# Optimization experiments

Hardware: AMD Instinct MI355X
Metric: run time of the kernel (lower is better)

## Reference

```python
import jax, jax.numpy as jnp
import numpy as np
from jax import lax

C = 64
B, H, W = 4, 192, 192


def conv2d(x, w, b):
    # x: [B,C,H,W], w: [O,I,3,3] (OIHW), stride 1, pad 1
    y = lax.conv_general_dilated(x, w, (1, 1), ((1, 1), (1, 1)),
                                 dimension_numbers=("NCHW", "OIHW", "NCHW"))
    return y + b[None, :, None, None]


def csm(x, w1, b1, w2, b2):
    # residual block: conv3x3 -> relu -> conv3x3 + skip
    return x + conv2d(jax.nn.relu(conv2d(x, w1, b1)), w2, b2)


def setup_inputs() -> dict:
    key = jax.random.key(0)
    ks = jax.random.split(key, 12)
    s = 1.0 / np.sqrt(C * 9)
    def cw(k):
        return jax.random.uniform(k, (C, C, 3, 3), jnp.float32, -s, s)
    def cb(k):
        return jax.random.uniform(k, (C,), jnp.float32, -s, s)
    return {
        "low1": jax.random.normal(ks[0], (B, C, H, W), jnp.float32),
        "low2": jax.random.normal(ks[1], (B, C, H, W), jnp.float32),
        "fe1_w1": cw(ks[2]), "fe1_b1": cb(ks[3]),
        "fe1_w2": cw(ks[4]), "fe1_b2": cb(ks[5]),
        "fe2_w1": cw(ks[6]), "fe2_b1": cb(ks[7]),
        "fe2_w2": cw(ks[8]), "fe2_b2": cb(ks[9]),
        "conv_w": cw(ks[10]), "conv_b": cb(ks[11]),
    }


def reference(low1, low2, fe1_w1, fe1_b1, fe1_w2, fe1_b2,
              fe2_w1, fe2_b1, fe2_w2, fe2_b2, conv_w, conv_b):
    Q1 = conv2d(csm(low1, fe1_w1, fe1_b1, fe1_w2, fe1_b2), conv_w, conv_b)
    K1 = conv2d(csm(low2, fe1_w1, fe1_b1, fe1_w2, fe1_b2), conv_w, conv_b)
    Q2 = conv2d(csm(low1, fe2_w1, fe2_b1, fe2_w2, fe2_b2), conv_w, conv_b)
    K2 = conv2d(csm(low2, fe2_w1, fe2_b1, fe2_w2, fe2_b2), conv_w, conv_b)

    # per-row cross-width scores: [B,H,W,W] (no scaling; softmax then relu)
    score1 = jax.nn.relu(jax.nn.softmax(jnp.einsum("bchw,bchv->bhwv", Q1, K1), axis=-1))
    score2 = jax.nn.relu(jax.nn.softmax(jnp.einsum("bchw,bchv->bhwv", Q2, K2), axis=-1))

    def apply_score(score, feat):
        # out[b,c,h,w] = sum_v score[b,h,w,v] * feat[b,c,h,v]
        return jnp.einsum("bhwv,bchv->bchw", score, feat)

    def apply_score_T(score, feat):
        # out[b,c,h,w] = sum_v score[b,h,v,w] * feat[b,c,h,v]
        return jnp.einsum("bhvw,bchv->bchw", score, feat)

    right2left1 = apply_score(score1, low2)
    right2left2 = apply_score(score2, low2)
    left2right1 = apply_score_T(score1, low1)
    left2right2 = apply_score_T(score2, low1)
    left2right2left = apply_score(score2, left2right1)
    right2left2right = apply_score_T(score2, right2left1)

    left = low1 + right2left1 + right2left2 + left2right2left
    right = low2 + left2right1 + left2right2 + right2left2right
    return (left, right)
```

## Files before the change

### kernel.cpp

```cpp
#include <hip/hip_runtime.h>
#include <stdint.h>

#define NB 4
#define NC 64
#define NH 192
#define NW 192

typedef __attribute__((ext_vector_type(8))) short bf16x8;
typedef __attribute__((ext_vector_type(4))) float f32x4;
typedef unsigned short u16;
typedef unsigned int u32;

__device__ inline float bf2f(u16 x){ u32 u = ((u32)x) << 16; return __builtin_bit_cast(float, u); }
__device__ inline u16 f2bf(float f){ u32 u = __builtin_bit_cast(u32, f); u32 r = u + 0x7fffu + ((u >> 16) & 1u); return (u16)(r >> 16); }
__device__ inline bf16x8 packf8(float4 a, float4 b){
  bf16x8 r;
  r[0]=(short)f2bf(a.x); r[1]=(short)f2bf(a.y); r[2]=(short)f2bf(a.z); r[3]=(short)f2bf(a.w);
  r[4]=(short)f2bf(b.x); r[5]=(short)f2bf(b.y); r[6]=(short)f2bf(b.z); r[7]=(short)f2bf(b.w);
  return r;
}

__global__ void wxform_k(const float* __restrict__ w0, const float* __restrict__ w1,
                         const float* __restrict__ w2, const float* __restrict__ w3,
                         const float* __restrict__ w4, u16* __restrict__ out){
  int idx = blockIdx.x * 256 + threadIdx.x;
  if (idx >= 5 * 36864) return;
  int t = idx / 36864, e = idx % 36864;
  int r = e >> 12, rem = e & 4095, co = rem >> 6, ci = rem & 63;
  const float* src = (t == 0) ? w0 : (t == 1) ? w1 : (t == 2) ? w2 : (t == 3) ? w3 : w4;
  out[idx] = f2bf(src[co * 576 + ci * 9 + r]);
}

__global__ __launch_bounds__(192) void nchw2nhwc_k(const float* __restrict__ in, u16* __restrict__ out){
  int bh = blockIdx.x; int b = bh / NH, h = bh % NH;
  int w = threadIdx.x;
  u16 v[64];
  const float* p = in + ((size_t)b * NC * NH + h) * NW + w;
#pragma unroll
  for (int c = 0; c < 64; ++c) v[c] = f2bf(p[(size_t)c * NH * NW]);
  uint4* q4 = (uint4*)(out + ((size_t)bh * NW + w) * NC);
#pragma unroll
  for (int i = 0; i < 8; ++i){
    uint4 t;
    t.x = (u32)v[i*8+0] | ((u32)v[i*8+1] << 16);
    t.y = (u32)v[i*8+2] | ((u32)v[i*8+3] << 16);
    t.z = (u32)v[i*8+4] | ((u32)v[i*8+5] << 16);
    t.w = (u32)v[i*8+6] | ((u32)v[i*8+7] << 16);
    q4[i] = t;
  }
}

__global__ __launch_bounds__(256) void bf2f_k(const u16* __restrict__ in, float* __restrict__ out){
  int i = blockIdx.x * 256 + threadIdx.x;
  uint4 v = ((const uint4*)in)[i];
  float4 f0, f1;
  f0.x = bf2f((u16)(v.x & 0xffff)); f0.y = bf2f((u16)(v.x >> 16));
  f0.z = bf2f((u16)(v.y & 0xffff)); f0.w = bf2f((u16)(v.y >> 16));
  f1.x = bf2f((u16)(v.z & 0xffff)); f1.y = bf2f((u16)(v.z >> 16));
  f1.z = bf2f((u16)(v.w & 0xffff)); f1.w = bf2f((u16)(v.w >> 16));
  ((float4*)out)[2*i]   = f0;
  ((float4*)out)[2*i+1] = f1;
}

__global__ __launch_bounds__(256) void conv3_k(const u16* __restrict__ in, const u16* __restrict__ wt,
    const float* __restrict__ bias, const u16* __restrict__ skip, u16* __restrict__ out, int relu){
  __shared__ __align__(16) u16 xr[3][98 * 72];
  int blk0 = blockIdx.x;
  int blk = (blk0 & 7) * 64 + (blk0 >> 3);
  int wh = blk & 1;
  int strip = blk >> 1;
  int g0 = strip * 3;
  int b = g0 / NH, h0 = g0 % NH;
  int wstart = wh * 96;
  int tid = threadIdx.x;
  int wvv = tid >> 6, lane = tid & 63, l15 = lane & 15, qd = lane >> 4;
  int mh = wvv >> 1, wq = wvv & 1;

#define STAGE(hh_) do { \
    int hh = (hh_); \
    int slot = ((hh % 3) + 3) % 3; \
    bool rowok = (hh >= 0) && (hh < NH); \
    const u16* src = in + (((size_t)b * NH + (rowok ? hh : 0)) * NW) * 64; \
    for (int k2 = tid; k2 < 784; k2 += 256){ \
      int x = k2 >> 3, part = k2 & 7; \
      int w = wstart - 1 + x; \
      uint4 val = make_uint4(0,0,0,0); \
      if (rowok && w >= 0 && w < NW) val = *(const uint4*)(src + (size_t)w * 64 + part * 8); \
      *(uint4*)&xr[slot][x * 72 + part * 8] = val; \
    } \
  } while(0)

  STAGE(h0 - 1);
  STAGE(h0);
  for (int j = 0; j < 3; ++j){
    int h = h0 + j;
    STAGE(h + 1);
    __syncthreads();
    f32x4 acc[2][3];
#pragma unroll
    for (int mt = 0; mt < 2; ++mt)
#pragma unroll
      for (int nt = 0; nt < 3; ++nt) acc[mt][nt] = (f32x4){0.f,0.f,0.f,0.f};
#pragma unroll
    for (int r = 0; r < 9; ++r){
      int ky = r / 3, kx = r % 3;
      int hs = h - 1 + ky;
      const u16* xbase = xr[((hs % 3) + 3) % 3];
#pragma unroll
      for (int ks = 0; ks < 2; ++ks){
        int ci = ks * 32 + qd * 8;
        const u16* wp_ = wt + r * 4096 + ci;
        bf16x8 a0 = *(const bf16x8*)(wp_ + (mh * 32 + l15) * 64);
        bf16x8 a1 = *(const bf16x8*)(wp_ + (mh * 32 + 16 + l15) * 64);
#pragma unroll
        for (int nt = 0; nt < 3; ++nt){
          int x = wq * 48 + nt * 16 + l15 + kx;
          bf16x8 bfr = *(const bf16x8*)&xbase[x * 72 + ci];
          acc[0][nt] = __builtin_amdgcn_mfma_f32_16x16x32_bf16(a0, bfr, acc[0][nt], 0, 0, 0);
          acc[1][nt] = __builtin_amdgcn_mfma_f32_16x16x32_bf16(a1, bfr, acc[1][nt], 0, 0, 0);
        }
      }
    }
    size_t rowbase = ((size_t)(b * NH + h)) * NW * 64;
#pragma unroll
    for (int mt = 0; mt < 2; ++mt){
      int co0 = mh * 32 + mt * 16 + qd * 4;
      float4 bb = *(const float4*)(bias + co0);
#pragma unroll
      for (int nt = 0; nt < 3; ++nt){
        int w = wstart + wq * 48 + nt * 16 + l15;
        size_t o = rowbase + (size_t)w * 64 + co0;
        float v0 = acc[mt][nt][0] + bb.x, v1 = acc[mt][nt][1] + bb.y;
        float v2 = acc[mt][nt][2] + bb.z, v3 = acc[mt][nt][3] + bb.w;
        if (relu){ v0 = fmaxf(v0,0.f); v1 = fmaxf(v1,0.f); v2 = fmaxf(v2,0.f); v3 = fmaxf(v3,0.f); }
        if (skip){
          uint2 ss = *(const uint2*)(skip + o);
          v0 += bf2f((u16)(ss.x & 0xffff)); v1 += bf2f((u16)(ss.x >> 16));
          v2 += bf2f((u16)(ss.y & 0xffff)); v3 += bf2f((u16)(ss.y >> 16));
        }
        uint2 st;
        st.x = (u32)f2bf(v0) | ((u32)f2bf(v1) << 16);
        st.y = (u32)f2bf(v2) | ((u32)f2bf(v3) << 16);
        *(uint2*)(out + o) = st;
      }
    }
    __syncthreads();
  }
#undef STAGE
}

template<int XYF32>
__global__ __launch_bounds__(256) void attn_k(const u16* __restrict__ Q, const u16* __restrict__ K,
    const void* __restrict__ Xv, const void* __restrict__ Yv,
    u16* __restrict__ outA, u16* __restrict__ outB){
  __shared__ __align__(16) u16 P[192 * 200];
  int bh = blockIdx.x, b = bh / NH, h = bh % NH;
  int tid = threadIdx.x, wv = tid >> 6, lane = tid & 63, l15 = lane & 15, qd = lane >> 4;
  size_t rowo = (size_t)bh * NW * 64;
  const u16* Qr = Q + rowo; const u16* Kr = K + rowo;
  const size_t CS = (size_t)NH * NW;
  size_t xb0 = (size_t)b * 64 * CS + (size_t)h * NW;
  const float* Xf = (const float*)Xv; const float* Yf = (const float*)Yv;
  const u16* Xb = (const u16*)Xv; const u16* Yb = (const u16*)Yv;

#pragma unroll 1
  for (int mi = 0; mi < 3; ++mi){
    int mt = wv * 3 + mi;
    f32x4 s[12];
#pragma unroll
    for (int nt = 0; nt < 12; ++nt) s[nt] = (f32x4){0,0,0,0};
#pragma unroll
    for (int ks = 0; ks < 2; ++ks){
      bf16x8 aq = *(const bf16x8*)(Qr + (mt * 16 + l15) * 64 + ks * 32 + qd * 8);
#pragma unroll
      for (int nt = 0; nt < 12; ++nt){
        bf16x8 bk = *(const bf16x8*)(Kr + (nt * 16 + l15) * 64 + ks * 32 + qd * 8);
        s[nt] = __builtin_amdgcn_mfma_f32_16x16x32_bf16(aq, bk, s[nt], 0, 0, 0);
      }
    }
#pragma unroll
    for (int rg = 0; rg < 4; ++rg){
      float mx = -1e30f;
#pragma unroll
      for (int nt = 0; nt < 12; ++nt) mx = fmaxf(mx, s[nt][rg]);
      mx = fmaxf(mx, __shfl_xor(mx, 1));
      mx = fmaxf(mx, __shfl_xor(mx, 2));
      mx = fmaxf(mx, __shfl_xor(mx, 4));
      mx = fmaxf(mx, __shfl_xor(mx, 8));
      float sum = 0.f;
#pragma unroll
      for (int nt = 0; nt < 12; ++nt){ float ev = __expf(s[nt][rg] - mx); s[nt][rg] = ev; sum += ev; }
      sum += __shfl_xor(sum, 1);
      sum += __shfl_xor(sum, 2);
      sum += __shfl_xor(sum, 4);
      sum += __shfl_xor(sum, 8);
      float inv = 1.f / sum;
      int w = mt * 16 + qd * 4 + rg;
#pragma unroll
      for (int nt = 0; nt < 12; ++nt){
        P[w * 200 + nt * 16 + l15] = f2bf(s[nt][rg] * inv);
      }
    }
  }

  {
    f32x4 accA[3][4];
#pragma unroll
    for (int ni = 0; ni < 3; ++ni)
#pragma unroll
      for (int mt = 0; mt < 4; ++mt) accA[ni][mt] = (f32x4){0,0,0,0};
#pragma unroll 1
    for (int ks = 0; ks < 6; ++ks){
      int v0 = ks * 32 + qd * 8;
      bf16x8 aX[4];
#pragma unroll
      for (int mt = 0; mt < 4; ++mt){
        int c = mt * 16 + l15;
        size_t off = xb0 + (size_t)c * CS + v0;
        if (XYF32){
          float4 x0 = *(const float4*)(Xf + off), x1 = *(const float4*)(Xf + off + 4);
          aX[mt] = packf8(x0, x1);
        } else {
          aX[mt] = *(const bf16x8*)(Xb + off);
        }
      }
#pragma unroll
      for (int ni = 0; ni < 3; ++ni){
        int wrow = (wv * 3 + ni) * 16 + l15;
        bf16x8 bP = *(const bf16x8*)&P[wrow * 200 + v0];
#pragma unroll
        for (int mt = 0; mt < 4; ++mt){
          accA[ni][mt] = __builtin_amdgcn_mfma_f32_16x16x32_bf16(aX[mt], bP, accA[ni][mt], 0, 0, 0);
        }
      }
    }
#pragma unroll
    for (int ni = 0; ni < 3; ++ni){
      int w = (wv * 3 + ni) * 16 + l15;
#pragma unroll
      for (int mt = 0; mt < 4; ++mt){
#pragma unroll
        for (int rg = 0; rg < 4; ++rg){
          int c = mt * 16 + qd * 4 + rg;
          size_t o = xb0 + (size_t)c * CS + w;
          float ra = XYF32 ? Yf[o] : bf2f(Yb[o]);
          outA[o] = f2bf(accA[ni][mt][rg] + ra);
        }
      }
    }
  }

  __syncthreads();

  {
    int r = tid >> 4, c = tid & 15;
#pragma unroll 1
    for (int TI = 0; TI < 12; ++TI){
      if (c > r){
        u16 a = P[(TI*16 + r)*200 + TI*16 + c];
        u16 d = P[(TI*16 + c)*200 + TI*16 + r];
        P[(TI*16 + r)*200 + TI*16 + c] = d;
        P[(TI*16 + c)*200 + TI*16 + r] = a;
      }
      int TJ = TI + 1;
      for (; TJ + 1 < 12; TJ += 2){
        u16 a0 = P[(TI*16 + r)*200 + TJ*16 + c];
        u16 b0 = P[(TJ*16 + c)*200 + TI*16 + r];
        u16 a1 = P[(TI*16 + r)*200 + (TJ+1)*16 + c];
        u16 b1 = P[((TJ+1)*16 + c)*200 + TI*16 + r];
        P[(TI*16 + r)*200 + TJ*16 + c] = b0;
        P[(TJ*16 + c)*200 + TI*16 + r] = a0;
        P[(TI*16 + r)*200 + (TJ+1)*16 + c] = b1;
        P[((TJ+1)*16 + c)*200 + TI*16 + r] = a1;
      }
      if (TJ < 12){
        u16 a0 = P[(TI*16 + r)*200 + TJ*16 + c];
        u16 b0 = P[(TJ*16 + c)*200 + TI*16 + r];
        P[(TI*16 + r)*200 + TJ*16 + c] = b0;
        P[(TJ*16 + c)*200 + TI*16 + r] = a0;
      }
    }
  }

  __syncthreads();

  {
    f32x4 accB[3][4];
#pragma unroll
    for (int ni = 0; ni < 3; ++ni)
#pragma unroll
      for (int mt = 0; mt < 4; ++mt) accB[ni][mt] = (f32x4){0,0,0,0};
#pragma unroll 1
    for (int ks = 0; ks < 6; ++ks){
      int v0 = ks * 32 + qd * 8;
      bf16x8 aY[4];
#pragma unroll
      for (int mt = 0; mt < 4; ++mt){
        int c = mt * 16 + l15;
        size_t off = xb0 + (size_t)c * CS + v0;
        if (XYF32){
          float4 y0 = *(const float4*)(Yf + off), y1 = *(const float4*)(Yf + off + 4);
          aY[mt] = packf8(y0, y1);
        } else {
          aY[mt] = *(const bf16x8*)(Yb + off);
        }
      }
#pragma unroll
      for (int ni = 0; ni < 3; ++ni){
        int wrow = (wv * 3 + ni) * 16 + l15;
        bf16x8 bPt = *(const bf16x8*)&P[wrow * 200 + v0];
#pragma unroll
        for (int mt = 0; mt < 4; ++mt){
          accB[ni][mt] = __builtin_amdgcn_mfma_f32_16x16x32_bf16(aY[mt], bPt, accB[ni][mt], 0, 0, 0);
        }
      }
    }
#pragma unroll
    for (int ni = 0; ni < 3; ++ni){
      int w = (wv * 3 + ni) * 16 + l15;
#pragma unroll
      for (int mt = 0; mt < 4; ++mt){
#pragma unroll
        for (int rg = 0; rg < 4; ++rg){
          int c = mt * 16 + qd * 4 + rg;
          size_t o = xb0 + (size_t)c * CS + w;
          float rb = XYF32 ? Xf[o] : bf2f(Xb[o]);
          outB[o] = f2bf(accB[ni][mt][rg] + rb);
        }
      }
    }
  }
}

extern "C" void kernel_launch(void* const* d_in, const int* in_sizes, int n_in,
                              void* d_out, int out_size, void* d_ws, size_t ws_size,
                              hipStream_t stream){
  const float* low1 = (const float*)d_in[0];
  const float* low2 = (const float*)d_in[1];
  const float* b11 = (const float*)d_in[3];
  const float* b12 = (const float*)d_in[5];
  const float* b21 = (const float*)d_in[7];
  const float* b22 = (const float*)d_in[9];
  const float* bcv = (const float*)d_in[11];
  const size_t BUF = (size_t)NB * NH * NW * NC;
  u16* WT = (u16*)d_ws;
  u16* s1 = WT + 184320;
  u16* s2 = s1 + BUF;
  u16* o1 = (u16*)d_out;
  u16* o2 = o1 + BUF;
  u16* o3 = o1 + 2 * BUF;
  u16* o4 = o1 + 3 * BUF;
  float* outL = (float*)d_out;
  float* outR = outL + BUF;

  wxform_k<<<dim3(720), dim3(256), 0, stream>>>(
      (const float*)d_in[2], (const float*)d_in[4], (const float*)d_in[6],
      (const float*)d_in[8], (const float*)d_in[10], WT);
  nchw2nhwc_k<<<dim3(NB * NH), dim3(192), 0, stream>>>(low1, o1);
  nchw2nhwc_k<<<dim3(NB * NH), dim3(192), 0, stream>>>(low2, o2);

#define CONV(in_, wti, bias_, skip_, out_, relu_) \
  conv3_k<<<dim3(512), dim3(256), 0, stream>>>(in_, WT + (wti) * 36864, bias_, skip_, out_, relu_)

  CONV(o1, 0, b11, (const u16*)nullptr, o3, 1);
  CONV(o3, 1, b12, o1, o4, 0);
  CONV(o4, 4, bcv, (const u16*)nullptr, s1, 0);
  CONV(o2, 0, b11, (const u16*)nullptr, o3, 1);
  CONV(o3, 1, b12, o2, o4, 0);
  CONV(o4, 4, bcv, (const u16*)nullptr, s2, 0);
  attn_k<1><<<dim3(NB * NH), dim3(256), 0, stream>>>(s1, s2, (const void*)low2, (const void*)low1, o3, o4);
  CONV(o1, 2, b21, (const u16*)nullptr, s1, 1);
  CONV(s1, 3, b22, o1, s2, 0);
  CONV(s2, 4, bcv, (const u16*)nullptr, o1, 0);
  CONV(o2, 2, b21, (const u16*)nullptr, s1, 1);
  CONV(s1, 3, b22, o2, s2, 0);
  CONV(s2, 4, bcv, (const u16*)nullptr, o2, 0);
  attn_k<0><<<dim3(NB * NH), dim3(256), 0, stream>>>(o1, o2, (const void*)o4, (const void*)o3, s1, s2);
  bf2f_k<<<dim3((int)(BUF / 8 / 256)), dim3(256), 0, stream>>>(s1, outL);
  bf2f_k<<<dim3((int)(BUF / 8 / 256)), dim3(256), 0, stream>>>(s2, outR);
#undef CONV
}
```

Baseline: 604.3 us.

## Drop LDS row staging in conv; one output row per block, read inputs from global

The conv kernel no longer stages three input rows into shared memory with barriers. Each block now computes a single output row half, and the MFMA B fragments load directly from global memory with boundary masking. The grid triples to 1536 blocks and launch bounds request 4 blocks per CU. This removes the LDS traffic and __syncthreads stalls and raises occupancy, but gives up the reuse of staged rows across 3 output rows and kx shifts, so it leans more on L1/L2 for the repeated loads.

Measured after the change: 1.288 ms. 113% more time.

```diff
diff --git a/kernel.cpp b/kernel.cpp
--- a/kernel.cpp
+++ b/kernel.cpp
@@ -62,50 +62,34 @@
   ((float4*)out)[2*i+1] = f1;
 }
 
-__global__ __launch_bounds__(256) void conv3_k(const u16* __restrict__ in, const u16* __restrict__ wt,
+__global__ __launch_bounds__(256, 4) void conv3_k(const u16* __restrict__ in, const u16* __restrict__ wt,
     const float* __restrict__ bias, const u16* __restrict__ skip, u16* __restrict__ out, int relu){
-  __shared__ __align__(16) u16 xr[3][98 * 72];
   int blk0 = blockIdx.x;
-  int blk = (blk0 & 7) * 64 + (blk0 >> 3);
+  int blk = (blk0 & 7) * 192 + (blk0 >> 3);
   int wh = blk & 1;
-  int strip = blk >> 1;
-  int g0 = strip * 3;
-  int b = g0 / NH, h0 = g0 % NH;
+  int bh = blk >> 1;
+  int b = bh / NH, h = bh % NH;
   int wstart = wh * 96;
   int tid = threadIdx.x;
-  int wvv = tid >> 6, lane = tid & 63, l15 = lane & 15, qd = lane >> 4;
-  int mh = wvv >> 1, wq = wvv & 1;
-
-#define STAGE(hh_) do { \
-    int hh = (hh_); \
-    int slot = ((hh % 3) + 3) % 3; \
-    bool rowok = (hh >= 0) && (hh < NH); \
-    const u16* src = in + (((size_t)b * NH + (rowok ? hh : 0)) * NW) * 64; \
-    for (int k2 = tid; k2 < 784; k2 += 256){ \
-      int x = k2 >> 3, part = k2 & 7; \
-      int w = wstart - 1 + x; \
-      uint4 val = make_uint4(0,0,0,0); \
-      if (rowok && w >= 0 && w < NW) val = *(const uint4*)(src + (size_t)w * 64 + part * 8); \
-      *(uint4*)&xr[slot][x * 72 + part * 8] = val; \
-    } \
-  } while(0)
-
-  STAGE(h0 - 1);
-  STAGE(h0);
-  for (int j = 0; j < 3; ++j){
-    int h = h0 + j;
-    STAGE(h + 1);
-    __syncthreads();
-    f32x4 acc[2][3];
-#pragma unroll
-    for (int mt = 0; mt < 2; ++mt)
-#pragma unroll
-      for (int nt = 0; nt < 3; ++nt) acc[mt][nt] = (f32x4){0.f,0.f,0.f,0.f};
-#pragma unroll
-    for (int r = 0; r < 9; ++r){
-      int ky = r / 3, kx = r % 3;
-      int hs = h - 1 + ky;
-      const u16* xbase = xr[((hs % 3) + 3) % 3];
+  int wv = tid >> 6, lane = tid & 63, l15 = lane & 15, qd = lane >> 4;
+  int mh = wv >> 1, wq = wv & 1;
+
+  f32x4 acc[2][3];
+#pragma unroll
+  for (int mt = 0; mt < 2; ++mt)
+#pragma unroll
+    for (int nt = 0; nt < 3; ++nt) acc[mt][nt] = (f32x4){0.f,0.f,0.f,0.f};
+
+  const bf16x8 zero8 = {0,0,0,0,0,0,0,0};
+
+#pragma unroll 1
+  for (int ky = 0; ky < 3; ++ky){
+    int hs = h - 1 + ky;
+    bool rowok = (hs >= 0) && (hs < NH);
+    const u16* srow = in + (((size_t)b * NH + (rowok ? hs : 0)) * NW) * 64;
+#pragma unroll
+    for (int kx = 0; kx < 3; ++kx){
+      int r = ky * 3 + kx;
 #pragma unroll
       for (int ks = 0; ks < 2; ++ks){
         int ci = ks * 32 + qd * 8;
@@ -114,39 +98,39 @@
         bf16x8 a1 = *(const bf16x8*)(wp_ + (mh * 32 + 16 + l15) * 64);
 #pragma unroll
         for (int nt = 0; nt < 3; ++nt){
-          int x = wq * 48 + nt * 16 + l15 + kx;
-          bf16x8 bfr = *(const bf16x8*)&xbase[x * 72 + ci];
+          int x = wstart + wq * 48 + nt * 16 + l15 + kx - 1;
+          bf16x8 bfr = zero8;
+          if (rowok && x >= 0 && x < NW) bfr = *(const bf16x8*)(srow + (size_t)x * 64 + ci);
           acc[0][nt] = __builtin_amdgcn_mfma_f32_16x16x32_bf16(a0, bfr, acc[0][nt], 0, 0, 0);
           acc[1][nt] = __builtin_amdgcn_mfma_f32_16x16x32_bf16(a1, bfr, acc[1][nt], 0, 0, 0);
         }
       }
     }
-    size_t rowbase = ((size_t)(b * NH + h)) * NW * 64;
-#pragma unroll
-    for (int mt = 0; mt < 2; ++mt){
-      int co0 = mh * 32 + mt * 16 + qd * 4;
-      float4 bb = *(const float4*)(bias + co0);
-#pragma unroll
-      for (int nt = 0; nt < 3; ++nt){
-        int w = wstart + wq * 48 + nt * 16 + l15;
-        size_t o = rowbase + (size_t)w * 64 + co0;
-        float v0 = acc[mt][nt][0] + bb.x, v1 = acc[mt][nt][1] + bb.y;
-        float v2 = acc[mt][nt][2] + bb.z, v3 = acc[mt][nt][3] + bb.w;
-        if (relu){ v0 = fmaxf(v0,0.f); v1 = fmaxf(v1,0.f); v2 = fmaxf(v2,0.f); v3 = fmaxf(v3,0.f); }
-        if (skip){
-          uint2 ss = *(const uint2*)(skip + o);
-          v0 += bf2f((u16)(ss.x & 0xffff)); v1 += bf2f((u16)(ss.x >> 16));
-          v2 += bf2f((u16)(ss.y & 0xffff)); v3 += bf2f((u16)(ss.y >> 16));
-        }
-        uint2 st;
-        st.x = (u32)f2bf(v0) | ((u32)f2bf(v1) << 16);
-        st.y = (u32)f2bf(v2) | ((u32)f2bf(v3) << 16);
-        *(uint2*)(out + o) = st;
-      }
-    }
-    __syncthreads();
-  }
-#undef STAGE
+  }
+
+  size_t rowbase = ((size_t)(b * NH + h)) * NW * 64;
+#pragma unroll
+  for (int mt = 0; mt < 2; ++mt){
+    int co0 = mh * 32 + mt * 16 + qd * 4;
+    float4 bb = *(const float4*)(bias + co0);
+#pragma unroll
+    for (int nt = 0; nt < 3; ++nt){
+      int w = wstart + wq * 48 + nt * 16 + l15;
+      size_t o = rowbase + (size_t)w * 64 + co0;
+      float v0 = acc[mt][nt][0] + bb.x, v1 = acc[mt][nt][1] + bb.y;
+      float v2 = acc[mt][nt][2] + bb.z, v3 = acc[mt][nt][3] + bb.w;
+      if (relu){ v0 = fmaxf(v0,0.f); v1 = fmaxf(v1,0.f); v2 = fmaxf(v2,0.f); v3 = fmaxf(v3,0.f); }
+      if (skip){
+        uint2 ss = *(const uint2*)(skip + o);
+        v0 += bf2f((u16)(ss.x & 0xffff)); v1 += bf2f((u16)(ss.x >> 16));
+        v2 += bf2f((u16)(ss.y & 0xffff)); v3 += bf2f((u16)(ss.y >> 16));
+      }
+      uint2 st;
+      st.x = (u32)f2bf(v0) | ((u32)f2bf(v1) << 16);
+      st.y = (u32)f2bf(v2) | ((u32)f2bf(v3) << 16);
+      *(uint2*)(out + o) = st;
+    }
+  }
 }
 
 template<int XYF32>
@@ -360,7 +344,7 @@
   nchw2nhwc_k<<<dim3(NB * NH), dim3(192), 0, stream>>>(low2, o2);
 
 #define CONV(in_, wti, bias_, skip_, out_, relu_) \
-  conv3_k<<<dim3(512), dim3(256), 0, stream>>>(in_, WT + (wti) * 36864, bias_, skip_, out_, relu_)
+  conv3_k<<<dim3(1536), dim3(256), 0, stream>>>(in_, WT + (wti) * 36864, bias_, skip_, out_, relu_)
 
   CONV(o1, 0, b11, (const u16*)nullptr, o3, 1);
   CONV(o3, 1, b12, o1, o4, 0);
```

## Batch paired conv streams into single launches and fuse attention epilogues

Applied to the files above, without the earlier changes.

The conv kernel now handles both feature streams (low1 and low2 paths) in one launch, with 768 blocks that each process 4 rows instead of 3. A launch-bounds occupancy hint of 3 blocks is added, and the number of conv launches drops from twelve to six. The attention kernel keeps both accumulator sets live and writes both outputs in one final epilogue, which allows outputs to alias inputs and lets buffers be reused. The aim is to cut launch overhead, improve GPU fill and amortize halo staging. The cost is more register pressure in the attention kernel and fewer blocks per stream.

New measurement: 671.0 us. 1.11x slower.

```diff
diff --git a/kernel.cpp b/kernel.cpp
--- a/kernel.cpp
+++ b/kernel.cpp
@@ -62,16 +62,24 @@
   ((float4*)out)[2*i+1] = f1;
 }
 
-__global__ __launch_bounds__(256) void conv3_k(const u16* __restrict__ in, const u16* __restrict__ wt,
-    const float* __restrict__ bias, const u16* __restrict__ skip, u16* __restrict__ out, int relu){
+__global__ __launch_bounds__(256, 3) void conv3m_k(
+    const u16* __restrict__ inA, const u16* __restrict__ inB,
+    const u16* __restrict__ wt, const float* __restrict__ bias,
+    const u16* __restrict__ skipA, const u16* __restrict__ skipB,
+    u16* __restrict__ outA, u16* __restrict__ outB, int relu){
   __shared__ __align__(16) u16 xr[3][98 * 72];
   int blk0 = blockIdx.x;
-  int blk = (blk0 & 7) * 64 + (blk0 >> 3);
-  int wh = blk & 1;
-  int strip = blk >> 1;
-  int g0 = strip * 3;
+  int blk = (blk0 & 7) * 96 + (blk0 >> 3);
+  int stream = blk / 384;
+  int r2 = blk % 384;
+  int wh = r2 & 1;
+  int strip = r2 >> 1;
+  int g0 = strip * 4;
   int b = g0 / NH, h0 = g0 % NH;
   int wstart = wh * 96;
+  const u16* in = stream ? inB : inA;
+  const u16* skip = stream ? skipB : skipA;
+  u16* out = stream ? outB : outA;
   int tid = threadIdx.x;
   int wvv = tid >> 6, lane = tid & 63, l15 = lane & 15, qd = lane >> 4;
   int mh = wvv >> 1, wq = wvv & 1;
@@ -92,7 +100,7 @@
 
   STAGE(h0 - 1);
   STAGE(h0);
-  for (int j = 0; j < 3; ++j){
+  for (int j = 0; j < 4; ++j){
     int h = h0 + j;
     STAGE(h + 1);
     __syncthreads();
@@ -203,49 +211,34 @@
     }
   }
 
-  {
-    f32x4 accA[3][4];
-#pragma unroll
-    for (int ni = 0; ni < 3; ++ni)
-#pragma unroll
-      for (int mt = 0; mt < 4; ++mt) accA[ni][mt] = (f32x4){0,0,0,0};
+  f32x4 accA[3][4], accB[3][4];
+#pragma unroll
+  for (int ni = 0; ni < 3; ++ni)
+#pragma unroll
+    for (int mt = 0; mt < 4; ++mt){ accA[ni][mt] = (f32x4){0,0,0,0}; accB[ni][mt] = (f32x4){0,0,0,0}; }
+
 #pragma unroll 1
-    for (int ks = 0; ks < 6; ++ks){
-      int v0 = ks * 32 + qd * 8;
-      bf16x8 aX[4];
+  for (int ks = 0; ks < 6; ++ks){
+    int v0 = ks * 32 + qd * 8;
+    bf16x8 aX[4];
+#pragma unroll
+    for (int mt = 0; mt < 4; ++mt){
+      int c = mt * 16 + l15;
+      size_t off = xb0 + (size_t)c * CS + v0;
+      if (XYF32){
+        float4 x0 = *(const float4*)(Xf + off), x1 = *(const float4*)(Xf + off + 4);
+        aX[mt] = packf8(x0, x1);
+      } else {
+        aX[mt] = *(const bf16x8*)(Xb + off);
+      }
+    }
+#pragma unroll
+    for (int ni = 0; ni < 3; ++ni){
+      int wrow = (wv * 3 + ni) * 16 + l15;
+      bf16x8 bP = *(const bf16x8*)&P[wrow * 200 + v0];
 #pragma unroll
       for (int mt = 0; mt < 4; ++mt){
-        int c = mt * 16 + l15;
-        size_t off = xb0 + (size_t)c * CS + v0;
-        if (XYF32){
-          float4 x0 = *(const float4*)(Xf + off), x1 = *(const float4*)(Xf + off + 4);
-          aX[mt] = packf8(x0, x1);
-        } else {
-          aX[mt] = *(const bf16x8*)(Xb + off);
-        }
-      }
-#pragma unroll
-      for (int ni = 0; ni < 3; ++ni){
-        int wrow = (wv * 3 + ni) * 16 + l15;
-        bf16x8 bP = *(const bf16x8*)&P[wrow * 200 + v0];
-#pragma unroll
-        for (int mt = 0; mt < 4; ++mt){
-          accA[ni][mt] = __builtin_amdgcn_mfma_f32_16x16x32_bf16(aX[mt], bP, accA[ni][mt], 0, 0, 0);
-        }
-      }
-    }
-#pragma unroll
-    for (int ni = 0; ni < 3; ++ni){
-      int w = (wv * 3 + ni) * 16 + l15;
-#pragma unroll
-      for (int mt = 0; mt < 4; ++mt){
-#pragma unroll
-        for (int rg = 0; rg < 4; ++rg){
-          int c = mt * 16 + qd * 4 + rg;
-          size_t o = xb0 + (size_t)c * CS + w;
-          float ra = XYF32 ? Yf[o] : bf2f(Yb[o]);
-          outA[o] = f2bf(accA[ni][mt][rg] + ra);
-        }
+        accA[ni][mt] = __builtin_amdgcn_mfma_f32_16x16x32_bf16(aX[mt], bP, accA[ni][mt], 0, 0, 0);
       }
     }
   }
@@ -284,49 +277,45 @@
 
   __syncthreads();
 
-  {
-    f32x4 accB[3][4];
-#pragma unroll
-    for (int ni = 0; ni < 3; ++ni)
-#pragma unroll
-      for (int mt = 0; mt < 4; ++mt) accB[ni][mt] = (f32x4){0,0,0,0};
 #pragma unroll 1
-    for (int ks = 0; ks < 6; ++ks){
-      int v0 = ks * 32 + qd * 8;
-      bf16x8 aY[4];
+  for (int ks = 0; ks < 6; ++ks){
+    int v0 = ks * 32 + qd * 8;
+    bf16x8 aY[4];
+#pragma unroll
+    for (int mt = 0; mt < 4; ++mt){
+      int c = mt * 16 + l15;
+      size_t off = xb0 + (size_t)c * CS + v0;
+      if (XYF32){
+        float4 y0 = *(const float4*)(Yf + off), y1 = *(const float4*)(Yf + off + 4);
+        aY[mt] = packf8(y0, y1);
+      } else {
+        aY[mt] = *(const bf16x8*)(Yb + off);
+      }
+    }
+#pragma unroll
+    for (int ni = 0; ni < 3; ++ni){
+      int wrow = (wv * 3 + ni) * 16 + l15;
+      bf16x8 bPt = *(const bf16x8*)&P[wrow * 200 + v0];
 #pragma unroll
       for (int mt = 0; mt < 4; ++mt){
-        int c = mt * 16 + l15;
-        size_t off = xb0 + (size_t)c * CS + v0;
-        if (XYF32){
-          float4 y0 = *(const float4*)(Yf + off), y1 = *(const float4*)(Yf + off + 4);
-          aY[mt] = packf8(y0, y1);
-        } else {
-          aY[mt] = *(const bf16x8*)(Yb + off);
-        }
-      }
-#pragma unroll
-      for (int ni = 0; ni < 3; ++ni){
-        int wrow = (wv * 3 + ni) * 16 + l15;
-        bf16x8 bPt = *(const bf16x8*)&P[wrow * 200 + v0];
-#pragma unroll
-        for (int mt = 0; mt < 4; ++mt){
-          accB[ni][mt] = __builtin_amdgcn_mfma_f32_16x16x32_bf16(aY[mt], bPt, accB[ni][mt], 0, 0, 0);
-        }
-      }
-    }
-#pragma unroll
-    for (int ni = 0; ni < 3; ++ni){
-      int w = (wv * 3 + ni) * 16 + l15;
-#pragma unroll
-      for (int mt = 0; mt < 4; ++mt){
-#pragma unroll
-        for (int rg = 0; rg < 4; ++rg){
-          int c = mt * 16 + qd * 4 + rg;
-          size_t o = xb0 + (size_t)c * CS + w;
-          float rb = XYF32 ? Xf[o] : bf2f(Xb[o]);
-          outB[o] = f2bf(accB[ni][mt][rg] + rb);
-        }
+        accB[ni][mt] = __builtin_amdgcn_mfma_f32_16x16x32_bf16(aY[mt], bPt, accB[ni][mt], 0, 0, 0);
+      }
+    }
+  }
+
+#pragma unroll
+  for (int ni = 0; ni < 3; ++ni){
+    int w = (wv * 3 + ni) * 16 + l15;
+#pragma unroll
+    for (int mt = 0; mt < 4; ++mt){
+#pragma unroll
+      for (int rg = 0; rg < 4; ++rg){
+        int c = mt * 16 + qd * 4 + rg;
+        size_t o = xb0 + (size_t)c * CS + w;
+        float ra = XYF32 ? Yf[o] : bf2f(Yb[o]);
+        float rb = XYF32 ? Xf[o] : bf2f(Xb[o]);
+        outA[o] = f2bf(accA[ni][mt][rg] + ra);
+        outB[o] = f2bf(accB[ni][mt][rg] + rb);
       }
     }
   }
@@ -359,24 +348,19 @@
   nchw2nhwc_k<<<dim3(NB * NH), dim3(192), 0, stream>>>(low1, o1);
   nchw2nhwc_k<<<dim3(NB * NH), dim3(192), 0, stream>>>(low2, o2);
 
-#define CONV(in_, wti, bias_, skip_, out_, relu_) \
-  conv3_k<<<dim3(512), dim3(256), 0, stream>>>(in_, WT + (wti) * 36864, bias_, skip_, out_, relu_)
-
-  CONV(o1, 0, b11, (const u16*)nullptr, o3, 1);
-  CONV(o3, 1, b12, o1, o4, 0);
-  CONV(o4, 4, bcv, (const u16*)nullptr, s1, 0);
-  CONV(o2, 0, b11, (const u16*)nullptr, o3, 1);
-  CONV(o3, 1, b12, o2, o4, 0);
-  CONV(o4, 4, bcv, (const u16*)nullptr, s2, 0);
-  attn_k<1><<<dim3(NB * NH), dim3(256), 0, stream>>>(s1, s2, (const void*)low2, (const void*)low1, o3, o4);
-  CONV(o1, 2, b21, (const u16*)nullptr, s1, 1);
-  CONV(s1, 3, b22, o1, s2, 0);
-  CONV(s2, 4, bcv, (const u16*)nullptr, o1, 0);
-  CONV(o2, 2, b21, (const u16*)nullptr, s1, 1);
-  CONV(s1, 3, b22, o2, s2, 0);
-  CONV(s2, 4, bcv, (const u16*)nullptr, o2, 0);
-  attn_k<0><<<dim3(NB * NH), dim3(256), 0, stream>>>(o1, o2, (const void*)o4, (const void*)o3, s1, s2);
+#define CONVM(inA_, inB_, wti, bias_, skA_, skB_, outA_, outB_, relu_) \
+  conv3m_k<<<dim3(768), dim3(256), 0, stream>>>(inA_, inB_, WT + (wti) * 36864, bias_, \
+                                                skA_, skB_, outA_, outB_, relu_)
+
+  CONVM(o1, o2, 0, b11, (const u16*)nullptr, (const u16*)nullptr, o3, o4, 1);
+  CONVM(o3, o4, 1, b12, o1, o2, s1, s2, 0);
+  CONVM(s1, s2, 4, bcv, (const u16*)nullptr, (const u16*)nullptr, o3, o4, 0);
+  attn_k<1><<<dim3(NB * NH), dim3(256), 0, stream>>>(o3, o4, (const void*)low2, (const void*)low1, s1, s2);
+  CONVM(o1, o2, 2, b21, (const u16*)nullptr, (const u16*)nullptr, o3, o4, 1);
+  CONVM(o3, o4, 3, b22, o1, o2, o1, o2, 0);
+  CONVM(o1, o2, 4, bcv, (const u16*)nullptr, (const u16*)nullptr, o3, o4, 0);
+  attn_k<0><<<dim3(NB * NH), dim3(256), 0, stream>>>(o3, o4, (const void*)s2, (const void*)s1, s1, s2);
   bf2f_k<<<dim3((int)(BUF / 8 / 256)), dim3(256), 0, stream>>>(s1, outL);
   bf2f_k<<<dim3((int)(BUF / 8 / 256)), dim3(256), 0, stream>>>(s2, outR);
-#undef CONV
-}
+#undef CONVM
+}
```
